# Performance work log

Hardware: AMD Instinct MI355X
Metric: run time of the kernel (lower is better)

## Reference

```python
import jax, jax.numpy as jnp
import numpy as np

HEADS = 16
DIM_HEAD = 64
SCALE = DIM_HEAD ** -0.5


def shift(x):
    # Transformer-XL relative shift trick. x: [..., i, j] -> [..., i, j]
    *pre, i, j = x.shape
    x = jnp.concatenate([x, jnp.zeros((*pre, i, i), x.dtype)], axis=-1)
    l = i + j - 1
    x = x.reshape(*pre, -1)
    pad = (-x.shape[-1]) % l
    x = jnp.concatenate([x, jnp.zeros((*pre, pad), x.dtype)], axis=-1)
    x = x.reshape(*pre, -1, l)
    return x[..., :i, i - 1:]


def setup_inputs() -> dict:
    key = jax.random.key(0)
    ks = jax.random.split(key, 8)
    b, t, e = 2, 1024, 1024
    mem_len, lmem_len = 1024, 128
    kv_len = t + mem_len + lmem_len
    return {
        "x": jax.random.normal(ks[0], (b, t, e), jnp.float32),
        "mem": jax.random.normal(ks[1], (b, mem_len, e), jnp.float32),
        "lmem": jax.random.normal(ks[2], (b, lmem_len, e), jnp.float32),
        "pos_emb": jax.random.normal(ks[3], (HEADS, kv_len, DIM_HEAD), jnp.float32),
        "input_mask": jnp.ones((b, t), bool),
        "Wq": jax.random.normal(ks[4], (e, e), jnp.float32) * 0.02,
        "Wkv": jax.random.normal(ks[5], (e, 2 * e), jnp.float32) * 0.02,
        "Wout": jax.random.normal(ks[6], (e, e), jnp.float32) * 0.02,
        "bout": jnp.zeros((e,), jnp.float32),
    }


def reference(x, mem, lmem, pos_emb, input_mask, Wq, Wkv, Wout, bout):
    b, t, e = x.shape
    h, dh = HEADS, DIM_HEAD
    mem_len, lmem_len = mem.shape[1], lmem.shape[1]
    total_mem = mem_len + lmem_len

    q = x @ Wq
    kv_input = jnp.concatenate([lmem, mem, x], axis=1)  # [b, kv_len, e]
    kv_len = kv_input.shape[1]
    k, v = jnp.split(kv_input @ Wkv, 2, axis=-1)

    def merge_heads(z):
        return z.reshape(b, -1, h, dh).transpose(0, 2, 1, 3)  # [b, h, n, dh]

    q, k, v = merge_heads(q), merge_heads(k), merge_heads(v)

    dots = jnp.einsum('bhid,bhjd->bhij', q, k) * SCALE  # [b, h, t, kv_len]

    pe = pos_emb[:, -kv_len:].astype(q.dtype)
    pos_dots = jnp.einsum('bhid,hjd->bhij', q, pe) * SCALE
    dots = dots + shift(pos_dots)

    mask_value = -jnp.finfo(dots.dtype).max

    pad_mask = input_mask[:, None, :, None] & input_mask[:, None, None, :]
    pad_mask = jnp.pad(pad_mask, ((0, 0), (0, 0), (0, 0), (total_mem, 0)), constant_values=True)
    dots = jnp.where(pad_mask, dots, mask_value)

    causal = jnp.triu(jnp.ones((t, t + total_mem), bool), k=1 + total_mem)
    dots = jnp.where(causal[None, None], mask_value, dots)

    attn = jax.nn.softmax(dots, axis=-1)
    out = jnp.einsum('bhij,bhjd->bhid', attn, v)
    out = out.transpose(0, 2, 1, 3).reshape(b, t, -1)
    return out @ Wout + bout
```

## Files before the change

kernel.cpp:

```cpp
#include <hip/hip_runtime.h>


typedef unsigned int   u32;
typedef unsigned short u16;
typedef unsigned long long u64;
typedef __attribute__((ext_vector_type(8))) short short8;
typedef __attribute__((ext_vector_type(4))) float f32x4;
typedef __attribute__((ext_vector_type(4))) u32   u32x4;

#define DEVI static __device__ __forceinline__
#define MFMA_BF16 __builtin_amdgcn_mfma_f32_16x16x32_bf16

DEVI u16 f2bf(float f) {
  u32 u = __builtin_bit_cast(u32, f);
  return (u16)((u + 0x7FFFu + ((u >> 16) & 1u)) >> 16);
}
DEVI float bf2f(u16 h) { u32 u = (u32)h << 16; return __builtin_bit_cast(float, u); }
DEVI u32 pk2(float lo, float hi) { return (u32)f2bf(lo) | ((u32)f2bf(hi) << 16); }
DEVI u32 cvtpk(float lo, float hi) {
  u32 r;
  asm("v_cvt_pk_bf16_f32 %0, %1, %2" : "=v"(r) : "v"(lo), "v"(hi));
  return r;
}

constexpr int T_ = 1024, E_ = 1024, KV = 2176, H_ = 16;
constexpr float QSCALE = 0.125f * 1.44269504088896f;

__global__ void k_prep_kvin(const float* __restrict__ x, const float* __restrict__ mem,
                            const float* __restrict__ lmem, u16* __restrict__ kvin) {
  int u = blockIdx.x * 256 + threadIdx.x;
  int b = u / (KV * E_ / 8);
  int r = u % (KV * E_ / 8);
  int j = r >> 7;
  int e8 = (r & 127) << 3;
  const float* src;
  if (j < 128)        src = lmem + ((size_t)(b * 128 + j) * E_ + e8);
  else if (j < 1152)  src = mem  + ((size_t)(b * 1024 + (j - 128)) * E_ + e8);
  else                src = x    + ((size_t)(b * 1024 + (j - 1152)) * E_ + e8);
  float4 a = ((const float4*)src)[0];
  float4 c = ((const float4*)src)[1];
  u32x4 o = { pk2(a.x, a.y), pk2(a.z, a.w), pk2(c.x, c.y), pk2(c.z, c.w) };
  *(u32x4*)(kvin + (size_t)u * 8) = o;
}

__global__ void k_prep_pe(const float* __restrict__ pos, u16* __restrict__ pe) {
  size_t u = (size_t)blockIdx.x * 256 + threadIdx.x;
  float4 a = ((const float4*)(pos + u * 8))[0];
  float4 c = ((const float4*)(pos + u * 8))[1];
  u32x4 o = { pk2(a.x, a.y), pk2(a.z, a.w), pk2(c.x, c.y), pk2(c.z, c.w) };
  *(u32x4*)(pe + u * 8) = o;
}

__global__ void k_transp(const float* __restrict__ src, u16* __restrict__ dst, int K, int N) {
  __shared__ float tile[32][33];
  int n0 = blockIdx.x * 32, k0 = blockIdx.y * 32;
  int tx = threadIdx.x, ty = threadIdx.y;
#pragma unroll
  for (int s = 0; s < 4; s++) tile[ty + 8 * s][tx] = src[(size_t)(k0 + ty + 8 * s) * N + n0 + tx];
  __syncthreads();
#pragma unroll
  for (int s = 0; s < 4; s++)
    dst[(size_t)(n0 + ty + 8 * s) * K + k0 + tx] = f2bf(tile[tx][ty + 8 * s]);
}

__global__ __launch_bounds__(256, 2)
void k_gemm_qkv(const u16* __restrict__ kvin, const u16* __restrict__ WallT,
                u16* __restrict__ qb, u16* __restrict__ kb, u16* __restrict__ vtb) {
  int bid = blockIdx.x;
  int b = bid / 336;
  int r = bid % 336;
  int nt, mt;
  if (r < 64) { nt = r >> 3; mt = 9 + (r & 7); }
  else { r -= 64; nt = 8 + r / 17; mt = r % 17; }

  const u16* A  = kvin + ((size_t)b * KV + (size_t)mt * 128) * E_;
  const u16* Bm = WallT + (size_t)nt * 128 * E_;

  __shared__ u16 As[2][128 * 40];
  __shared__ u16 Bs[2][128 * 40];

  int t = threadIdx.x;
  int wid = t >> 6, lane = t & 63;
  int wr = wid >> 1, wc = wid & 1;
  int l15 = lane & 15, l4 = lane >> 4;

  f32x4 acc[4][4] = {};
  int arow = t >> 2, aslot = t & 3;

  u32x4 ra[2], rb[2];
  auto ld = [&](int kt_) {
    int k0 = kt_ * 32;
#pragma unroll
    for (int p = 0; p < 2; p++) {
      ra[p] = *(const u32x4*)(A  + (size_t)(arow + 64 * p) * E_ + k0 + aslot * 8);
      rb[p] = *(const u32x4*)(Bm + (size_t)(arow + 64 * p) * E_ + k0 + aslot * 8);
    }
  };
  auto st = [&](int buf) {
#pragma unroll
    for (int p = 0; p < 2; p++) {
      *(u32x4*)(As[buf] + (arow + 64 * p) * 40 + aslot * 8) = ra[p];
      *(u32x4*)(Bs[buf] + (arow + 64 * p) * 40 + aslot * 8) = rb[p];
    }
  };

  ld(0); st(0); ld(1);
  for (int kt = 0; kt < 32; kt++) {
    __syncthreads();
    int buf = kt & 1;
    short8 af[4], bfv[4];
#pragma unroll
    for (int m = 0; m < 4; m++)
      af[m] = *(const short8*)(As[buf] + (wr * 64 + m * 16 + l15) * 40 + l4 * 8);
#pragma unroll
    for (int n = 0; n < 4; n++)
      bfv[n] = *(const short8*)(Bs[buf] + (wc * 64 + n * 16 + l15) * 40 + l4 * 8);
#pragma unroll
    for (int m = 0; m < 4; m++)
#pragma unroll
      for (int n = 0; n < 4; n++)
        acc[m][n] = MFMA_BF16(af[m], bfv[n], acc[m][n], 0, 0, 0);
    if (kt + 1 < 32) st(buf ^ 1);
    if (kt + 2 < 32) ld(kt + 2);
  }
  int grow_base = mt * 128 + wr * 64;
  int ncol_base = nt * 128 + wc * 64;
  if (nt < 8) {
#pragma unroll
    for (int m = 0; m < 4; m++)
#pragma unroll
      for (int n = 0; n < 4; n++) {
        int col = ncol_base + n * 16 + l15;
        int head = col >> 6, d = col & 63;
#pragma unroll
        for (int rg = 0; rg < 4; rg++) {
          int row = grow_base + m * 16 + l4 * 4 + rg - 1152;
          qb[(((size_t)b * 16 + head) * 1024 + row) * 64 + d] = f2bf(acc[m][n][rg] * QSCALE);
        }
      }
  } else if (nt < 16) {
#pragma unroll
    for (int m = 0; m < 4; m++)
#pragma unroll
      for (int n = 0; n < 4; n++) {
        int c = ncol_base + n * 16 + l15 - 1024;
        int head = c >> 6, d = c & 63;
#pragma unroll
        for (int rg = 0; rg < 4; rg++) {
          int row = grow_base + m * 16 + l4 * 4 + rg;
          kb[(((size_t)b * 16 + head) * KV + row) * 64 + d] = f2bf(acc[m][n][rg]);
        }
      }
  } else {
#pragma unroll
    for (int m = 0; m < 4; m++)
#pragma unroll
      for (int n = 0; n < 4; n++) {
        int c = ncol_base + n * 16 + l15 - 2048;
        int head = c >> 6, d = c & 63;
        int jb = grow_base + m * 16 + l4 * 4;
        u64 pv = (u64)f2bf(acc[m][n][0]) | ((u64)f2bf(acc[m][n][1]) << 16)
               | ((u64)f2bf(acc[m][n][2]) << 32) | ((u64)f2bf(acc[m][n][3]) << 48);
        *(u64*)(vtb + (((size_t)b * 16 + head) * 64 + d) * KV + jb) = pv;
      }
  }
}

__global__ __launch_bounds__(256, 2)
void k_attn(const u16* __restrict__ qb, const u16* __restrict__ kb,
            const u16* __restrict__ vtb, const u16* __restrict__ peb,
            u16* __restrict__ ao) {
  int bid = blockIdx.x;
  int xcd = bid & 7;
  int itr = (bid >> 3) & 15;
  int g   = bid >> 7;
  int it  = (g >= 2) ? (15 - itr) : itr;
  int bh = g * 8 + xcd;
  int b = bh >> 4, h = bh & 15;
  int i0 = it * 64;

  __shared__ u16 Klds[2][64][72];
  __shared__ u16 Vt[2][64][72];
  __shared__ u16 Band[64][136];
  __shared__ u16 Pb[4][16][72];

  int t = threadIdx.x, wid = t >> 6, lane = t & 63;
  int l15 = lane & 15, l4 = lane >> 4;
  int il = wid * 16 + l15;
  int srow = t >> 3, ssl = t & 7;

  const u16* kbase  = kb  + (size_t)bh * KV * 64;
  const u16* vtbase = vtb + (size_t)bh * 64 * KV;
  const u16* pebase = peb + (size_t)h * KV * 64;

  const u16* qptr = qb + ((size_t)bh * 1024 + i0 + il) * 64 + l4 * 8;
  short8 qf0 = *(const short8*)qptr;
  short8 qf1 = *(const short8*)(qptr + 32);

  f32x4 Of[4] = {};
  float mr = -1e30f, lr = 0.f;
  int njt = it + 19;

  u32x4 rk0, rk1, rv0, rv1;
  auto load_regs = [&](int jt_) {
    int j0_ = jt_ * 64;
    rk0 = *(const u32x4*)(kbase + (size_t)(j0_ + srow) * 64 + ssl * 8);
    rk1 = *(const u32x4*)(kbase + (size_t)(j0_ + srow + 32) * 64 + ssl * 8);
    rv0 = *(const u32x4*)(vtbase + (size_t)srow * KV + j0_ + ssl * 8);
    rv1 = *(const u32x4*)(vtbase + (size_t)(srow + 32) * KV + j0_ + ssl * 8);
  };
  auto store_tile = [&](int buf) {
    *(u32x4*)(&Klds[buf][srow][ssl * 8]) = rk0;
    *(u32x4*)(&Klds[buf][srow + 32][ssl * 8]) = rk1;
    *(u32x4*)(&Vt[buf][srow][ssl * 8]) = rv0;
    *(u32x4*)(&Vt[buf][srow + 32][ssl * 8]) = rv1;
  };
  auto load_pe = [&](int prb, short8* pf) {
#pragma unroll
    for (int rc = 0; rc < 4; rc++) {
      int rr = prb + rc * 16 + l15; rr = rr > 2175 ? 2175 : rr;
#pragma unroll
      for (int kk = 0; kk < 2; kk++)
        pf[rc * 2 + kk] = *(const short8*)(pebase + (size_t)rr * 64 + kk * 32 + l4 * 8);
    }
  };
  auto band_mfma_store = [&](int prb, const short8* pf) {
    f32x4 acc[4];
    __builtin_amdgcn_s_setprio(1);
#pragma unroll
    for (int rc = 0; rc < 4; rc++) {
      f32x4 a = {};
      a = MFMA_BF16(pf[rc * 2 + 0], qf0, a, 0, 0, 0);
      a = MFMA_BF16(pf[rc * 2 + 1], qf1, a, 0, 0, 0);
      acc[rc] = a;
    }
    __builtin_amdgcn_s_setprio(0);
#pragma unroll
    for (int rc = 0; rc < 4; rc++) {
      int rb = prb + rc * 16 + l4 * 4 + il + 1;
      u32 w01 = cvtpk(acc[rc][0], acc[rc][1]);
      u32 w23 = cvtpk(acc[rc][2], acc[rc][3]);
      Band[il][rb & 127]       = (u16)w01;
      Band[il][(rb + 1) & 127] = (u16)(w01 >> 16);
      Band[il][(rb + 2) & 127] = (u16)w23;
      Band[il][(rb + 3) & 127] = (u16)(w23 >> 16);
    }
  };

  load_regs(0);
  store_tile(0);
  short8 pf[8];
  load_pe(960 - i0, pf);
  band_mfma_store(960 - i0, pf);
  load_pe(1024 - i0, pf);
  load_regs(1);

  int cur = 0;
  for (int jt = 0; jt < njt; jt++) {
    bool domask = (jt == njt - 1);
    __syncthreads();

    f32x4 sc[4];
    __builtin_amdgcn_s_setprio(1);
#pragma unroll
    for (int jc = 0; jc < 4; jc++) {
      f32x4 a = {};
      short8 k0 = *(const short8*)(&Klds[cur][jc * 16 + l15][l4 * 8]);
      short8 k1 = *(const short8*)(&Klds[cur][jc * 16 + l15][32 + l4 * 8]);
      a = MFMA_BF16(k0, qf0, a, 0, 0, 0);
      a = MFMA_BF16(k1, qf1, a, 0, 0, 0);
      sc[jc] = a;
    }
    __builtin_amdgcn_s_setprio(0);

    band_mfma_store(1024 + 64 * jt - i0, pf);
    if (jt + 1 < njt) load_pe(1024 + 64 * (jt + 1) - i0, pf);

    short8 vf[8];
#pragma unroll
    for (int df = 0; df < 4; df++)
#pragma unroll
      for (int kk = 0; kk < 2; kk++)
        vf[df * 2 + kk] = *(const short8*)(&Vt[cur][df * 16 + l15][kk * 32 + l4 * 8]);

    asm volatile("s_waitcnt lgkmcnt(0)" ::: "memory");
    __builtin_amdgcn_sched_barrier(0);

    float P[4][4];
    float mx = -1e30f;
    int cb0 = ((jt - it) & 1) << 6;
#pragma unroll
    for (int jc = 0; jc < 4; jc++) {
      u64 bl = *(const u64*)(&Band[il][cb0 + jc * 16 + l4 * 4]);
#pragma unroll
      for (int rg = 0; rg < 4; rg++) {
        int jj = jc * 16 + l4 * 4 + rg;
        float v = sc[jc][rg] + bf2f((u16)(bl >> (16 * rg)));
        if (domask && (jj > il)) v = -1e30f;
        P[jc][rg] = v;
        mx = fmaxf(mx, v);
      }
    }
    mx = fmaxf(mx, __shfl_xor(mx, 16, 64));
    mx = fmaxf(mx, __shfl_xor(mx, 32, 64));
    if (!__all(mx <= mr + 8.0f)) {
      float mnew = fmaxf(mr, mx);
      float fac = exp2f(mr - mnew);
      mr = mnew;
      lr *= fac;
#pragma unroll
      for (int dc = 0; dc < 4; dc++) Of[dc] *= fac;
    }
    float ps = 0.f;
#pragma unroll
    for (int jc = 0; jc < 4; jc++)
#pragma unroll
      for (int rg = 0; rg < 4; rg++) {
        float p = exp2f(P[jc][rg] - mr);
        P[jc][rg] = p;
        ps += p;
      }
    ps += __shfl_xor(ps, 16, 64);
    ps += __shfl_xor(ps, 32, 64);
    lr += ps;

#pragma unroll
    for (int jc = 0; jc < 4; jc++) {
      int cb = jc * 16 + l4 * 4;
      *(u32*)(&Pb[wid][l15][cb])     = cvtpk(P[jc][0], P[jc][1]);
      *(u32*)(&Pb[wid][l15][cb + 2]) = cvtpk(P[jc][2], P[jc][3]);
    }
    asm volatile("s_waitcnt lgkmcnt(0)" ::: "memory");
    __builtin_amdgcn_sched_barrier(0);

    short8 pB0 = *(const short8*)(&Pb[wid][l15][l4 * 8]);
    short8 pB1 = *(const short8*)(&Pb[wid][l15][32 + l4 * 8]);
    __builtin_amdgcn_s_setprio(1);
#pragma unroll
    for (int df = 0; df < 4; df++) {
      Of[df] = MFMA_BF16(vf[df * 2 + 0], pB0, Of[df], 0, 0, 0);
      Of[df] = MFMA_BF16(vf[df * 2 + 1], pB1, Of[df], 0, 0, 0);
    }
    __builtin_amdgcn_s_setprio(0);

    if (jt + 1 < njt) {
      store_tile(cur ^ 1);
      if (jt + 2 < njt) load_regs(jt + 2);
    }
    cur ^= 1;
  }

  float inv = 1.0f / lr;
  size_t ob = ((size_t)b * 1024 + i0 + il) * 1024 + h * 64;
#pragma unroll
  for (int df = 0; df < 4; df++) {
    u64 pv = (u64)f2bf(Of[df][0] * inv)         | ((u64)f2bf(Of[df][1] * inv) << 16)
           | ((u64)f2bf(Of[df][2] * inv) << 32) | ((u64)f2bf(Of[df][3] * inv) << 48);
    *(u64*)(ao + ob + df * 16 + l4 * 4) = pv;
  }
}

__global__ __launch_bounds__(256, 2)
void k_gemm_out(const u16* __restrict__ ao, const u16* __restrict__ WoT,
                const float* __restrict__ bias, float* __restrict__ out) {
  int mt = blockIdx.x & 31, nt = blockIdx.x >> 5;
  const u16* A  = ao  + (size_t)mt * 64 * E_;
  const u16* Bm = WoT + (size_t)nt * 128 * E_;
  __shared__ u16 As[64 * 40];
  __shared__ u16 Bs[128 * 40];
  int t = threadIdx.x, wid = t >> 6, lane = t & 63;
  int wr = wid >> 1, wc = wid & 1, l15 = lane & 15, l4 = lane >> 4;
  f32x4 acc[2][4] = {};
  int arow = t >> 2, aslot = t & 3;

  u32x4 ra, rb[2];
  ra = *(const u32x4*)(A + (size_t)arow * E_ + aslot * 8);
#pragma unroll
  for (int p = 0; p < 2; p++)
    rb[p] = *(const u32x4*)(Bm + (size_t)(arow + 64 * p) * E_ + aslot * 8);
  for (int kt = 0; kt < 32; kt++) {
    __syncthreads();
    *(u32x4*)(As + arow * 40 + aslot * 8) = ra;
#pragma unroll
    for (int p = 0; p < 2; p++)
      *(u32x4*)(Bs + (arow + 64 * p) * 40 + aslot * 8) = rb[p];
    __syncthreads();
    if (kt + 1 < 32) {
      int k0 = (kt + 1) * 32;
      ra = *(const u32x4*)(A + (size_t)arow * E_ + k0 + aslot * 8);
#pragma unroll
      for (int p = 0; p < 2; p++)
        rb[p] = *(const u32x4*)(Bm + (size_t)(arow + 64 * p) * E_ + k0 + aslot * 8);
    }
    short8 af[2], bfv[4];
#pragma unroll
    for (int m = 0; m < 2; m++)
      af[m] = *(const short8*)(As + (wr * 32 + m * 16 + l15) * 40 + l4 * 8);
#pragma unroll
    for (int n = 0; n < 4; n++)
      bfv[n] = *(const short8*)(Bs + (wc * 64 + n * 16 + l15) * 40 + l4 * 8);
#pragma unroll
    for (int m = 0; m < 2; m++)
#pragma unroll
      for (int n = 0; n < 4; n++)
        acc[m][n] = MFMA_BF16(af[m], bfv[n], acc[m][n], 0, 0, 0);
  }
#pragma unroll
  for (int n = 0; n < 4; n++) {
    int col = nt * 128 + wc * 64 + n * 16 + l15;
    float bv = bias[col];
#pragma unroll
    for (int m = 0; m < 2; m++) {
      int row = mt * 64 + wr * 32 + m * 16 + l4 * 4;
#pragma unroll
      for (int rg = 0; rg < 4; rg++)
        out[(size_t)(row + rg) * E_ + col] = acc[m][n][rg] + bv;
    }
  }
}

extern "C" void kernel_launch(void* const* d_in, const int* in_sizes, int n_in,
                              void* d_out, int out_size, void* d_ws, size_t ws_size,
                              hipStream_t stream) {
  (void)in_sizes; (void)n_in; (void)out_size; (void)ws_size;
  const float* x    = (const float*)d_in[0];
  const float* mem  = (const float*)d_in[1];
  const float* lmem = (const float*)d_in[2];
  const float* pos  = (const float*)d_in[3];
  const float* Wq   = (const float*)d_in[5];
  const float* Wkv  = (const float*)d_in[6];
  const float* Wout = (const float*)d_in[7];
  const float* bout = (const float*)d_in[8];
  float* out = (float*)d_out;

  u16* kvin  = (u16*)d_ws;
  u16* pe    = kvin  + (size_t)2 * KV * E_;
  u16* WallT = pe    + (size_t)H_ * KV * 64;
  u16* WoT   = WallT + (size_t)3072 * E_;
  u16* qb    = WoT   + (size_t)E_ * E_;
  u16* kb    = qb    + (size_t)2 * H_ * T_ * 64;
  u16* vtb   = kb    + (size_t)2 * H_ * KV * 64;
  u16* ao    = vtb   + (size_t)2 * H_ * KV * 64;

  k_prep_kvin<<<2176, 256, 0, stream>>>(x, mem, lmem, kvin);
  k_prep_pe<<<1088, 256, 0, stream>>>(pos, pe);
  k_transp<<<dim3(32, 32), dim3(32, 8), 0, stream>>>(Wq,   WallT,             1024, 1024);
  k_transp<<<dim3(64, 32), dim3(32, 8), 0, stream>>>(Wkv,  WallT + 1024*1024, 1024, 2048);
  k_transp<<<dim3(32, 32), dim3(32, 8), 0, stream>>>(Wout, WoT,               1024, 1024);
  k_gemm_qkv<<<672, 256, 0, stream>>>(kvin, WallT, qb, kb, vtb);
  k_attn<<<512, 256, 0, stream>>>(qb, kb, vtb, pe, ao);
  k_gemm_out<<<256, 256, 0, stream>>>(ao, WoT, bout, out);
}
```

Measured before the change: 146.6 us.

## Split attention KV range across two blocks with merge kernel, shuffle P in registers

Each attention query tile's KV loop is split into two halves run by separate blocks, which write partial O, max and sum to workspace; a new merge kernel then combines them into the bf16 output. This is meant to double the grid and balance the uneven causal work. The P matrix is redistributed with lane shuffles instead of a round trip through LDS, launch bounds go up to 3 blocks per CU, and the output GEMM gains a double-buffered LDS pipeline that drops one barrier per iteration. The cost is extra fp32 partial traffic, one more kernel launch, and register pressure from the higher occupancy target.

```diff
diff --git a/kernel.cpp b/kernel.cpp
--- a/kernel.cpp
+++ b/kernel.cpp
@@ -166,23 +166,27 @@
   }
 }
 
-__global__ __launch_bounds__(256, 2)
+__global__ __launch_bounds__(256, 3)
 void k_attn(const u16* __restrict__ qb, const u16* __restrict__ kb,
             const u16* __restrict__ vtb, const u16* __restrict__ peb,
-            u16* __restrict__ ao) {
+            u16* __restrict__ ao, float* __restrict__ opart,
+            float* __restrict__ mlpart, int split) {
   int bid = blockIdx.x;
-  int xcd = bid & 7;
-  int itr = (bid >> 3) & 15;
-  int g   = bid >> 7;
-  int it  = (g >= 2) ? (15 - itr) : itr;
+  int xcd = bid & 7, bk = bid >> 3;
+  int half, itf, g;
+  if (split) { half = bk & 1; itf = (bk >> 1) & 15; g = bk >> 5; }
+  else       { half = 0;      itf = bk & 15;        g = bk >> 4; }
+  int it = 15 - itf;
   int bh = g * 8 + xcd;
   int b = bh >> 4, h = bh & 15;
   int i0 = it * 64;
+  int njt = it + 19;
+  int jt0 = 0, jt1 = njt;
+  if (split) { int mid = (njt + 1) >> 1; if (half) jt0 = mid; else jt1 = mid; }
 
   __shared__ u16 Klds[2][64][72];
   __shared__ u16 Vt[2][64][72];
-  __shared__ u16 Band[64][136];
-  __shared__ u16 Pb[4][16][72];
+  __shared__ u16 Band[64][132];
 
   int t = threadIdx.x, wid = t >> 6, lane = t & 63;
   int l15 = lane & 15, l4 = lane >> 4;
@@ -199,7 +203,10 @@
 
   f32x4 Of[4] = {};
   float mr = -1e30f, lr = 0.f;
-  int njt = it + 19;
+
+  int sA = l15 + (((2 * l4) & 3) << 4);
+  int sB = l15 + (((2 * l4 + 1) & 3) << 4);
+  bool hiSel = (l4 & 2);
 
   u32x4 rk0, rk1, rv0, rv1;
   auto load_regs = [&](int jt_) {
@@ -247,16 +254,16 @@
     }
   };
 
-  load_regs(0);
+  load_regs(jt0);
   store_tile(0);
   short8 pf[8];
-  load_pe(960 - i0, pf);
-  band_mfma_store(960 - i0, pf);
-  load_pe(1024 - i0, pf);
-  load_regs(1);
+  load_pe(960 + 64 * jt0 - i0, pf);
+  band_mfma_store(960 + 64 * jt0 - i0, pf);
+  load_pe(1024 + 64 * jt0 - i0, pf);
+  load_regs(jt0 + 1);
 
   int cur = 0;
-  for (int jt = 0; jt < njt; jt++) {
+  for (int jt = jt0; jt < jt1; jt++) {
     bool domask = (jt == njt - 1);
     __syncthreads();
 
@@ -274,7 +281,7 @@
     __builtin_amdgcn_s_setprio(0);
 
     band_mfma_store(1024 + 64 * jt - i0, pf);
-    if (jt + 1 < njt) load_pe(1024 + 64 * (jt + 1) - i0, pf);
+    if (jt + 1 < jt1) load_pe(1024 + 64 * (jt + 1) - i0, pf);
 
     short8 vf[8];
 #pragma unroll
@@ -312,51 +319,97 @@
       for (int dc = 0; dc < 4; dc++) Of[dc] *= fac;
     }
     float ps = 0.f;
-#pragma unroll
-    for (int jc = 0; jc < 4; jc++)
+    u32 p01[4], p23[4];
+#pragma unroll
+    for (int jc = 0; jc < 4; jc++) {
 #pragma unroll
       for (int rg = 0; rg < 4; rg++) {
         float p = exp2f(P[jc][rg] - mr);
         P[jc][rg] = p;
         ps += p;
       }
+      p01[jc] = cvtpk(P[jc][0], P[jc][1]);
+      p23[jc] = cvtpk(P[jc][2], P[jc][3]);
+    }
     ps += __shfl_xor(ps, 16, 64);
     ps += __shfl_xor(ps, 32, 64);
     lr += ps;
 
-#pragma unroll
-    for (int jc = 0; jc < 4; jc++) {
-      int cb = jc * 16 + l4 * 4;
-      *(u32*)(&Pb[wid][l15][cb])     = cvtpk(P[jc][0], P[jc][1]);
-      *(u32*)(&Pb[wid][l15][cb + 2]) = cvtpk(P[jc][2], P[jc][3]);
-    }
-    asm volatile("s_waitcnt lgkmcnt(0)" ::: "memory");
-    __builtin_amdgcn_sched_barrier(0);
-
-    short8 pB0 = *(const short8*)(&Pb[wid][l15][l4 * 8]);
-    short8 pB1 = *(const short8*)(&Pb[wid][l15][32 + l4 * 8]);
     __builtin_amdgcn_s_setprio(1);
 #pragma unroll
+    for (int kk = 0; kk < 2; kk++) {
+      int jA = 2 * kk, jB = 2 * kk + 1;
+      u32 a0 = (u32)__shfl((int)p01[jA], sA, 64), a0h = (u32)__shfl((int)p01[jB], sA, 64);
+      u32 a1 = (u32)__shfl((int)p23[jA], sA, 64), a1h = (u32)__shfl((int)p23[jB], sA, 64);
+      u32 a2 = (u32)__shfl((int)p01[jA], sB, 64), a2h = (u32)__shfl((int)p01[jB], sB, 64);
+      u32 a3 = (u32)__shfl((int)p23[jA], sB, 64), a3h = (u32)__shfl((int)p23[jB], sB, 64);
+      u32x4 pw = { hiSel ? a0h : a0, hiSel ? a1h : a1,
+                   hiSel ? a2h : a2, hiSel ? a3h : a3 };
+      short8 pB = __builtin_bit_cast(short8, pw);
+#pragma unroll
+      for (int df = 0; df < 4; df++)
+        Of[df] = MFMA_BF16(vf[df * 2 + kk], pB, Of[df], 0, 0, 0);
+    }
+    __builtin_amdgcn_s_setprio(0);
+
+    if (jt + 1 < jt1) {
+      store_tile(cur ^ 1);
+      if (jt + 2 < jt1) load_regs(jt + 2);
+    }
+    cur ^= 1;
+  }
+
+  if (split) {
+    int part = (bh * 16 + it) * 2 + half;
+    float* Op = opart + (size_t)part * 4096;
+#pragma unroll
+    for (int df = 0; df < 4; df++)
+      *(f32x4*)(Op + il * 64 + df * 16 + l4 * 4) = Of[df];
+    if (l4 == 0) {
+      mlpart[part * 128 + il * 2]     = mr;
+      mlpart[part * 128 + il * 2 + 1] = lr;
+    }
+  } else {
+    float inv = 1.0f / lr;
+    size_t ob = ((size_t)b * 1024 + i0 + il) * 1024 + h * 64;
+#pragma unroll
     for (int df = 0; df < 4; df++) {
-      Of[df] = MFMA_BF16(vf[df * 2 + 0], pB0, Of[df], 0, 0, 0);
-      Of[df] = MFMA_BF16(vf[df * 2 + 1], pB1, Of[df], 0, 0, 0);
-    }
-    __builtin_amdgcn_s_setprio(0);
-
-    if (jt + 1 < njt) {
-      store_tile(cur ^ 1);
-      if (jt + 2 < njt) load_regs(jt + 2);
-    }
-    cur ^= 1;
-  }
-
-  float inv = 1.0f / lr;
-  size_t ob = ((size_t)b * 1024 + i0 + il) * 1024 + h * 64;
-#pragma unroll
-  for (int df = 0; df < 4; df++) {
-    u64 pv = (u64)f2bf(Of[df][0] * inv)         | ((u64)f2bf(Of[df][1] * inv) << 16)
-           | ((u64)f2bf(Of[df][2] * inv) << 32) | ((u64)f2bf(Of[df][3] * inv) << 48);
-    *(u64*)(ao + ob + df * 16 + l4 * 4) = pv;
+      u64 pv = (u64)f2bf(Of[df][0] * inv)         | ((u64)f2bf(Of[df][1] * inv) << 16)
+             | ((u64)f2bf(Of[df][2] * inv) << 32) | ((u64)f2bf(Of[df][3] * inv) << 48);
+      *(u64*)(ao + ob + df * 16 + l4 * 4) = pv;
+    }
+  }
+}
+
+__global__ __launch_bounds__(256)
+void k_merge(const float* __restrict__ opart, const float* __restrict__ mlpart,
+             u16* __restrict__ ao) {
+  int p = blockIdx.x;
+  int bh = p >> 4, it = p & 15;
+  int b = bh >> 4, h = bh & 15;
+  int t = threadIdx.x;
+  int r = t >> 2, c = t & 3;
+  const float* A = opart + ((size_t)p * 2) * 4096 + r * 64 + c * 16;
+  const float* B = A + 4096;
+  float mA = mlpart[(p * 2) * 128 + r * 2],     lA = mlpart[(p * 2) * 128 + r * 2 + 1];
+  float mB = mlpart[(p * 2 + 1) * 128 + r * 2], lB = mlpart[(p * 2 + 1) * 128 + r * 2 + 1];
+  float M = fmaxf(mA, mB);
+  float wA = exp2f(mA - M), wB = exp2f(mB - M);
+  float inv = 1.0f / (wA * lA + wB * lB);
+  wA *= inv; wB *= inv;
+  size_t ob = ((size_t)b * 1024 + it * 64 + r) * 1024 + h * 64 + c * 16;
+#pragma unroll
+  for (int s = 0; s < 2; s++) {
+    f32x4 va0 = *(const f32x4*)(A + s * 8);
+    f32x4 va1 = *(const f32x4*)(A + s * 8 + 4);
+    f32x4 vb0 = *(const f32x4*)(B + s * 8);
+    f32x4 vb1 = *(const f32x4*)(B + s * 8 + 4);
+    u32x4 o;
+    o[0] = pk2(va0[0] * wA + vb0[0] * wB, va0[1] * wA + vb0[1] * wB);
+    o[1] = pk2(va0[2] * wA + vb0[2] * wB, va0[3] * wA + vb0[3] * wB);
+    o[2] = pk2(va1[0] * wA + vb1[0] * wB, va1[1] * wA + vb1[1] * wB);
+    o[3] = pk2(va1[2] * wA + vb1[2] * wB, va1[3] * wA + vb1[3] * wB);
+    *(u32x4*)(ao + ob + s * 8) = o;
   }
 }
 
@@ -366,44 +419,46 @@
   int mt = blockIdx.x & 31, nt = blockIdx.x >> 5;
   const u16* A  = ao  + (size_t)mt * 64 * E_;
   const u16* Bm = WoT + (size_t)nt * 128 * E_;
-  __shared__ u16 As[64 * 40];
-  __shared__ u16 Bs[128 * 40];
+  __shared__ u16 As[2][64 * 40];
+  __shared__ u16 Bs[2][128 * 40];
   int t = threadIdx.x, wid = t >> 6, lane = t & 63;
   int wr = wid >> 1, wc = wid & 1, l15 = lane & 15, l4 = lane >> 4;
   f32x4 acc[2][4] = {};
   int arow = t >> 2, aslot = t & 3;
 
   u32x4 ra, rb[2];
-  ra = *(const u32x4*)(A + (size_t)arow * E_ + aslot * 8);
-#pragma unroll
-  for (int p = 0; p < 2; p++)
-    rb[p] = *(const u32x4*)(Bm + (size_t)(arow + 64 * p) * E_ + aslot * 8);
+  auto ld = [&](int kt_) {
+    int k0 = kt_ * 32;
+    ra = *(const u32x4*)(A + (size_t)arow * E_ + k0 + aslot * 8);
+#pragma unroll
+    for (int p = 0; p < 2; p++)
+      rb[p] = *(const u32x4*)(Bm + (size_t)(arow + 64 * p) * E_ + k0 + aslot * 8);
+  };
+  auto st = [&](int buf) {
+    *(u32x4*)(As[buf] + arow * 40 + aslot * 8) = ra;
+#pragma unroll
+    for (int p = 0; p < 2; p++)
+      *(u32x4*)(Bs[buf] + (arow + 64 * p) * 40 + aslot * 8) = rb[p];
+  };
+
+  ld(0); st(0); ld(1);
   for (int kt = 0; kt < 32; kt++) {
     __syncthreads();
-    *(u32x4*)(As + arow * 40 + aslot * 8) = ra;
-#pragma unroll
-    for (int p = 0; p < 2; p++)
-      *(u32x4*)(Bs + (arow + 64 * p) * 40 + aslot * 8) = rb[p];
-    __syncthreads();
-    if (kt + 1 < 32) {
-      int k0 = (kt + 1) * 32;
-      ra = *(const u32x4*)(A + (size_t)arow * E_ + k0 + aslot * 8);
-#pragma unroll
-      for (int p = 0; p < 2; p++)
-        rb[p] = *(const u32x4*)(Bm + (size_t)(arow + 64 * p) * E_ + k0 + aslot * 8);
-    }
+    int buf = kt & 1;
     short8 af[2], bfv[4];
 #pragma unroll
     for (int m = 0; m < 2; m++)
-      af[m] = *(const short8*)(As + (wr * 32 + m * 16 + l15) * 40 + l4 * 8);
+      af[m] = *(const short8*)(As[buf] + (wr * 32 + m * 16 + l15) * 40 + l4 * 8);
 #pragma unroll
     for (int n = 0; n < 4; n++)
-      bfv[n] = *(const short8*)(Bs + (wc * 64 + n * 16 + l15) * 40 + l4 * 8);
+      bfv[n] = *(const short8*)(Bs[buf] + (wc * 64 + n * 16 + l15) * 40 + l4 * 8);
 #pragma unroll
     for (int m = 0; m < 2; m++)
 #pragma unroll
       for (int n = 0; n < 4; n++)
         acc[m][n] = MFMA_BF16(af[m], bfv[n], acc[m][n], 0, 0, 0);
+    if (kt + 1 < 32) st(buf ^ 1);
+    if (kt + 2 < 32) ld(kt + 2);
   }
 #pragma unroll
   for (int n = 0; n < 4; n++) {
@@ -422,7 +477,7 @@
 extern "C" void kernel_launch(void* const* d_in, const int* in_sizes, int n_in,
                               void* d_out, int out_size, void* d_ws, size_t ws_size,
                               hipStream_t stream) {
-  (void)in_sizes; (void)n_in; (void)out_size; (void)ws_size;
+  (void)in_sizes; (void)n_in; (void)out_size;
   const float* x    = (const float*)d_in[0];
   const float* mem  = (const float*)d_in[1];
   const float* lmem = (const float*)d_in[2];
@@ -441,6 +496,12 @@
   u16* kb    = qb    + (size_t)2 * H_ * T_ * 64;
   u16* vtb   = kb    + (size_t)2 * H_ * KV * 64;
   u16* ao    = vtb   + (size_t)2 * H_ * KV * 64;
+  float* opart  = (float*)(ao + (size_t)2048 * 1024);
+  float* mlpart = opart + (size_t)1024 * 4096;
+
+  size_t base_bytes = (size_t)((char*)(ao + (size_t)2048 * 1024) - (char*)d_ws);
+  size_t needed = base_bytes + (size_t)1024 * 4096 * 4 + (size_t)1024 * 128 * 4;
+  int split = (ws_size >= needed) ? 1 : 0;
 
   k_prep_kvin<<<2176, 256, 0, stream>>>(x, mem, lmem, kvin);
   k_prep_pe<<<1088, 256, 0, stream>>>(pos, pe);
@@ -448,6 +509,7 @@
   k_transp<<<dim3(64, 32), dim3(32, 8), 0, stream>>>(Wkv,  WallT + 1024*1024, 1024, 2048);
   k_transp<<<dim3(32, 32), dim3(32, 8), 0, stream>>>(Wout, WoT,               1024, 1024);
   k_gemm_qkv<<<672, 256, 0, stream>>>(kvin, WallT, qb, kb, vtb);
-  k_attn<<<512, 256, 0, stream>>>(qb, kb, vtb, pe, ao);
+  k_attn<<<split ? 1024 : 512, 256, 0, stream>>>(qb, kb, vtb, pe, ao, opart, mlpart, split);
+  if (split) k_merge<<<512, 256, 0, stream>>>(opart, mlpart, ao);
   k_gemm_out<<<256, 256, 0, stream>>>(ao, WoT, bout, out);
 }
```

Result: slower. 166.6 us, median of 2 (+13.7%).
